# Kernel optimization log

Measured on AMD Instinct MI355X. Metric: run time of the kernel, lower is better.

Reference implementation:

```python
import jax, jax.numpy as jnp
import numpy as np

EPS = 1e-5

def _act_quant(x):
    # per-token int8 absmax quantization with straight-through estimator
    scale = 127.0 / jnp.clip(jnp.max(jnp.abs(x), axis=-1, keepdims=True), EPS, None)
    q = jnp.clip(jnp.round(x * scale), -128.0, 127.0) / scale
    return x + jax.lax.stop_gradient(q - x)

def _weight_quant(w):
    # per-tensor ternary (1.58-bit) quantization with STE
    scale = 1.0 / jnp.clip(jnp.mean(jnp.abs(w)), EPS, None)
    q = jnp.clip(jnp.round(w * scale), -1.0, 1.0) / scale
    return w + jax.lax.stop_gradient(q - w)

def _bitlinear(x, w, b):
    y = jnp.einsum('bsd,od->bso', _act_quant(x), _weight_quant(w))
    return y + b

def setup_inputs() -> dict:
    key = jax.random.key(0)
    k1, k2, k3, k4, k5 = jax.random.split(key, 5)
    B, S, D, F = 8, 4096, 1024, 3072
    return {
        'x': jax.random.normal(k1, (B, S, D), dtype=jnp.float32),
        'up_w': jax.random.normal(k2, (F, D), dtype=jnp.float32) * 0.125,
        'up_b': jax.random.normal(k3, (F,), dtype=jnp.float32) * 0.01,
        'down_w': jax.random.normal(k4, (D, F), dtype=jnp.float32) * 0.125,
        'down_b': jax.random.normal(k5, (D,), dtype=jnp.float32) * 0.01,
    }

def reference(x, up_w, up_b, down_w, down_b):
    hidden = _bitlinear(x, up_w, up_b)          # [B,S,3072]
    hidden = jnp.square(jax.nn.relu(hidden))    # relu(h)^2
    return _bitlinear(hidden, down_w, down_b)   # [B,S,1024]
```

## Files before the change

kernel.cpp:

```cpp
#include <hip/hip_runtime.h>
#include <hip/hip_bf16.h>
#include <stdint.h>

#define EPS 1e-5f

typedef int v4i __attribute__((ext_vector_type(4)));
typedef int v16i __attribute__((ext_vector_type(16)));
typedef const __attribute__((address_space(1))) void g_void;
typedef __attribute__((address_space(3))) void l_void;

__device__ inline float block_max_nw(float v, int nw) {
    __shared__ float s[8];
#pragma unroll
    for (int o = 32; o; o >>= 1) v = fmaxf(v, __shfl_xor(v, o, 64));
    if ((threadIdx.x & 63) == 0) s[threadIdx.x >> 6] = v;
    __syncthreads();
    float m = s[0];
    for (int i = 1; i < nw; ++i) m = fmaxf(m, s[i]);
    return m;
}

__device__ inline float block_sum64x4(float v) {
    __shared__ float s[4];
#pragma unroll
    for (int o = 32; o; o >>= 1) v += __shfl_xor(v, o, 64);
    if ((threadIdx.x & 63) == 0) s[threadIdx.x >> 6] = v;
    __syncthreads();
    return s[0] + s[1] + s[2] + s[3];
}

__global__ __launch_bounds__(256) void abs_sum_part_k(const float4* __restrict__ w,
                                                      int n4, float* __restrict__ part) {
    float s = 0.0f;
    for (int i = blockIdx.x * 256 + threadIdx.x; i < n4; i += 1024 * 256) {
        float4 v = w[i];
        s += fabsf(v.x) + fabsf(v.y) + fabsf(v.z) + fabsf(v.w);
    }
    s = block_sum64x4(s);
    if (threadIdx.x == 0) part[blockIdx.x] = s;
}

__global__ __launch_bounds__(256) void abs_sum_final_k(const float* __restrict__ parts,
                                                       float* __restrict__ sums) {
    const float* p = parts + blockIdx.x * 1024;
    const int t = threadIdx.x;
    float s = p[t] + p[t + 256] + p[t + 512] + p[t + 768];
    s = block_sum64x4(s);
    if (t == 0) sums[blockIdx.x] = s;
}

__global__ __launch_bounds__(256) void wquant_k(const float4* __restrict__ w,
                                                char4* __restrict__ q,
                                                const float* __restrict__ sum) {
    const float mean = fmaxf(sum[0] * (1.0f / 3145728.0f), EPS);
    const float scale = 1.0f / mean;
    const int i = blockIdx.x * 256 + threadIdx.x;
    float4 v = w[i];
    char4 c;
    c.x = (signed char)(int)fmaxf(fminf(rintf(v.x * scale), 1.0f), -1.0f);
    c.y = (signed char)(int)fmaxf(fminf(rintf(v.y * scale), 1.0f), -1.0f);
    c.z = (signed char)(int)fmaxf(fminf(rintf(v.z * scale), 1.0f), -1.0f);
    c.w = (signed char)(int)fmaxf(fminf(rintf(v.w * scale), 1.0f), -1.0f);
    q[i] = c;
}

__global__ __launch_bounds__(256) void aquant_k(const float4* __restrict__ x,
                                                char4* __restrict__ q,
                                                float* __restrict__ deq) {
    const int row = blockIdx.x, t = threadIdx.x;
    const float4 v = x[(size_t)row * 256 + t];
    float m = fmaxf(fmaxf(fabsf(v.x), fabsf(v.y)), fmaxf(fabsf(v.z), fabsf(v.w)));
    m = block_max_nw(m, 4);
    const float mc = fmaxf(m, EPS);
    const float sc = 127.0f / mc;
    char4 c;
    c.x = (signed char)(int)fmaxf(fminf(rintf(v.x * sc), 127.0f), -128.0f);
    c.y = (signed char)(int)fmaxf(fminf(rintf(v.y * sc), 127.0f), -128.0f);
    c.z = (signed char)(int)fmaxf(fminf(rintf(v.z * sc), 127.0f), -128.0f);
    c.w = (signed char)(int)fmaxf(fminf(rintf(v.w * sc), 127.0f), -128.0f);
    q[(size_t)row * 256 + t] = c;
    if (t == 0) deq[row] = mc / 127.0f;
}

__global__ __launch_bounds__(384) void hquant_k(unsigned short* __restrict__ hid,
                                                float* __restrict__ deq) {
    const size_t row = blockIdx.x;
    const int t = threadIdx.x;
    unsigned short* rp = hid + row * 3072;
    const uint4 u = ((const uint4*)rp)[t];
    float v[8];
    {
        uint32_t uu[4] = {u.x, u.y, u.z, u.w};
#pragma unroll
        for (int i = 0; i < 4; ++i) {
            uint32_t lo = uu[i] << 16, hi = uu[i] & 0xFFFF0000u;
            v[2 * i]     = __uint_as_float(lo);
            v[2 * i + 1] = __uint_as_float(hi);
        }
    }
    float m = 0.0f;
#pragma unroll
    for (int i = 0; i < 8; ++i) m = fmaxf(m, fabsf(v[i]));
    m = block_max_nw(m, 6);
    const float mc = fmaxf(m, EPS);
    const float sc = 127.0f / mc;
    uint32_t p0 = 0, p1 = 0;
#pragma unroll
    for (int i = 0; i < 4; ++i) {
        int c = (int)fminf(rintf(v[i] * sc), 127.0f);
        p0 |= (uint32_t)(c & 255) << (8 * i);
    }
#pragma unroll
    for (int i = 0; i < 4; ++i) {
        int c = (int)fminf(rintf(v[4 + i] * sc), 127.0f);
        p1 |= (uint32_t)(c & 255) << (8 * i);
    }
    uint2 pk; pk.x = p0; pk.y = p1;
    ((uint2*)rp)[t] = pk;
    if (t == 0) deq[row] = mc / 127.0f;
}

template <bool RELU2, typename OutT>
__global__ __launch_bounds__(512, 2) void gemm_i8(
    const int8_t* __restrict__ A, int lda,
    const int8_t* __restrict__ B, int ldb,
    OutT* __restrict__ O, int ldo,
    const float* __restrict__ rowDeq,
    const float* __restrict__ sumPtr,
    const float* __restrict__ bias,
    int K, int nTiles) {
    __shared__ __align__(16) char As[2][32768];
    __shared__ __align__(16) char Bs[2][32768];
    const int t = threadIdx.x;
    const int lane = t & 63;
    const int w = t >> 6;
    const int wm = w >> 2;
    const int wn = w & 3;
    const int xcd = blockIdx.x & 7;
    const int sb = blockIdx.x >> 3;
    const int bm = xcd + 8 * (sb / nTiles);
    const int bn = sb % nTiles;
    const long m0 = (long)bm * 256;
    const long n0 = (long)bn * 256;

    v16i acc[4][2];
#pragma unroll
    for (int i = 0; i < 4; ++i)
#pragma unroll
        for (int j = 0; j < 2; ++j) acc[i][j] = (v16i)(0);

    const int r32 = lane & 31;
    const int h = lane >> 5;
    const int swz = r32 & 7;
    const int srow = lane >> 3;
    const int scol = ((lane & 7) ^ srow) * 16;
    const int mloc = wm * 128;
    const int nloc = wn * 64;

    const int8_t* pa = A + (m0 + w * 8 + srow) * (long)lda + scol;
    const int8_t* pb = B + (n0 + w * 8 + srow) * (long)ldb + scol;

    int cs[4];
#pragma unroll
    for (int ks = 0; ks < 4; ++ks) cs[ks] = ((ks * 2 + h) ^ swz) * 16;

    const int NT = K >> 7;

    auto STAGE = [&](int tt, int buf) {
        const long ko = (long)tt << 7;
#pragma unroll
        for (int r = 0; r < 4; ++r)
            __builtin_amdgcn_global_load_lds((g_void*)(pa + (long)(r * 64) * lda + ko),
                                             (l_void*)(As[buf] + r * 8192 + w * 1024), 16, 0, 0);
#pragma unroll
        for (int r = 0; r < 4; ++r)
            __builtin_amdgcn_global_load_lds((g_void*)(pb + (long)(r * 64) * ldb + ko),
                                             (l_void*)(Bs[buf] + r * 8192 + w * 1024), 16, 0, 0);
    };

    STAGE(0, 0);
    STAGE(1, 1);
    asm volatile("s_waitcnt vmcnt(8)" ::: "memory");
    __builtin_amdgcn_s_barrier();
    asm volatile("" ::: "memory");

    for (int tt = 0; tt < NT; ++tt) {
        const int cur = tt & 1;
        v4i af[4][4], bf[2][4];
#pragma unroll
        for (int ks = 0; ks < 4; ++ks) {
#pragma unroll
            for (int mt = 0; mt < 4; ++mt)
                af[mt][ks] = *(const v4i*)(As[cur] + (mloc + mt * 32 + r32) * 128 + cs[ks]);
#pragma unroll
            for (int nt = 0; nt < 2; ++nt)
                bf[nt][ks] = *(const v4i*)(Bs[cur] + (nloc + nt * 32 + r32) * 128 + cs[ks]);
        }
        asm volatile("s_waitcnt lgkmcnt(0)" ::: "memory");
        __builtin_amdgcn_s_barrier();
        asm volatile("" ::: "memory");
        const bool pf = (tt + 2 < NT);
        if (pf) STAGE(tt + 2, cur);
        __builtin_amdgcn_s_setprio(1);
#pragma unroll
        for (int ks = 0; ks < 4; ++ks)
#pragma unroll
            for (int mt = 0; mt < 4; ++mt)
#pragma unroll
                for (int nt = 0; nt < 2; ++nt)
                    acc[mt][nt] = __builtin_amdgcn_mfma_i32_32x32x32_i8(
                        af[mt][ks], bf[nt][ks], acc[mt][nt], 0, 0, 0);
        __builtin_amdgcn_s_setprio(0);
        if (pf) asm volatile("s_waitcnt vmcnt(8)" ::: "memory");
        else    asm volatile("s_waitcnt vmcnt(0)" ::: "memory");
        __builtin_amdgcn_s_barrier();
        asm volatile("" ::: "memory");
    }

    const float wdeq = fmaxf(sumPtr[0] * (1.0f / 3145728.0f), EPS);
#pragma unroll
    for (int mt = 0; mt < 4; ++mt) {
#pragma unroll
        for (int g = 0; g < 4; ++g) {
#pragma unroll
            for (int rr = 0; rr < 4; ++rr) {
                const long row = m0 + mloc + mt * 32 + g * 8 + h * 4 + rr;
                const float rs = rowDeq[row] * wdeq;
#pragma unroll
                for (int nt = 0; nt < 2; ++nt) {
                    const long col = n0 + nloc + nt * 32 + r32;
                    float val = (float)acc[mt][nt][g * 4 + rr] * rs + bias[col];
                    if (RELU2) {
                        val = fmaxf(val, 0.0f);
                        val = val * val;
                    }
                    O[row * (long)ldo + col] = (OutT)val;
                }
            }
        }
    }
}

extern "C" void kernel_launch(void* const* d_in, const int* in_sizes, int n_in,
                              void* d_out, int out_size, void* d_ws, size_t ws_size,
                              hipStream_t stream) {
    const float* x      = (const float*)d_in[0];
    const float* up_w   = (const float*)d_in[1];
    const float* up_b   = (const float*)d_in[2];
    const float* down_w = (const float*)d_in[3];
    const float* down_b = (const float*)d_in[4];

    char* ws = (char*)d_ws;
    float*  sums   = (float*)ws;
    float*  parts  = (float*)(ws + 256);
    int8_t* qw_dn  = (int8_t*)(ws + 256 + 8192);
    float*  deqh   = (float*)(ws + 256 + 8192 + 3145728);
    __hip_bfloat16* hidden = (__hip_bfloat16*)(ws + 256 + 8192 + 3145728 + 131072);

    int8_t* qx    = (int8_t*)d_out;
    int8_t* qw_up = qx + 33554432;
    float*  deqx  = (float*)(qx + 33554432 + 3145728);

    abs_sum_part_k<<<1024, 256, 0, stream>>>((const float4*)up_w, 786432, parts);
    abs_sum_part_k<<<1024, 256, 0, stream>>>((const float4*)down_w, 786432, parts + 1024);
    abs_sum_final_k<<<2, 256, 0, stream>>>(parts, sums);

    wquant_k<<<3072, 256, 0, stream>>>((const float4*)up_w, (char4*)qw_up, &sums[0]);
    wquant_k<<<3072, 256, 0, stream>>>((const float4*)down_w, (char4*)qw_dn, &sums[1]);
    aquant_k<<<32768, 256, 0, stream>>>((const float4*)x, (char4*)qx, deqx);

    gemm_i8<true, __hip_bfloat16><<<1536, 512, 0, stream>>>(
        qx, 1024, qw_up, 1024, hidden, 3072, deqx, &sums[0], up_b, 1024, 12);
    hquant_k<<<32768, 384, 0, stream>>>((unsigned short*)hidden, deqh);
    gemm_i8<false, float><<<512, 512, 0, stream>>>(
        (const int8_t*)hidden, 6144, qw_dn, 3072, (float*)d_out, 1024,
        deqh, &sums[1], down_b, 3072, 4);
}
```

Before: 582.3 us.

## Switch int8 GEMM to 4-stage K=64 pipeline with single barrier per step

Changes the int8 GEMM main loop from double-buffered K=128 tiles to four LDS buffers of K=64 tiles, issuing the prefetch three stages ahead. The LDS layout and XOR swizzle are redone for 64-byte rows. The mid-iteration barrier after the LDS reads is dropped, so each step has only one barrier. The aim is deeper latency hiding of global loads and less synchronisation. The cost is twice as many loop iterations, with less MFMA work between barriers.

```diff
diff --git a/kernel.cpp b/kernel.cpp
--- a/kernel.cpp
+++ b/kernel.cpp
@@ -129,8 +129,8 @@
     const float* __restrict__ sumPtr,
     const float* __restrict__ bias,
     int K, int nTiles) {
-    __shared__ __align__(16) char As[2][32768];
-    __shared__ __align__(16) char Bs[2][32768];
+    __shared__ __align__(16) char As[4][16384];
+    __shared__ __align__(16) char Bs[4][16384];
     const int t = threadIdx.x;
     const int lane = t & 63;
     const int w = t >> 6;
@@ -151,59 +151,63 @@
 
     const int r32 = lane & 31;
     const int h = lane >> 5;
-    const int swz = r32 & 7;
-    const int srow = lane >> 3;
-    const int scol = ((lane & 7) ^ srow) * 16;
-    const int mloc = wm * 128;
-    const int nloc = wn * 64;
-
-    const int8_t* pa = A + (m0 + w * 8 + srow) * (long)lda + scol;
-    const int8_t* pb = B + (n0 + w * 8 + srow) * (long)ldb + scol;
-
-    int cs[4];
-#pragma unroll
-    for (int ks = 0; ks < 4; ++ks) cs[ks] = ((ks * 2 + h) ^ swz) * 16;
-
-    const int NT = K >> 7;
-
-    auto STAGE = [&](int tt, int buf) {
-        const long ko = (long)tt << 7;
-#pragma unroll
-        for (int r = 0; r < 4; ++r)
-            __builtin_amdgcn_global_load_lds((g_void*)(pa + (long)(r * 64) * lda + ko),
-                                             (l_void*)(As[buf] + r * 8192 + w * 1024), 16, 0, 0);
-#pragma unroll
-        for (int r = 0; r < 4; ++r)
-            __builtin_amdgcn_global_load_lds((g_void*)(pb + (long)(r * 64) * ldb + ko),
-                                             (l_void*)(Bs[buf] + r * 8192 + w * 1024), 16, 0, 0);
+
+    const int srow = lane >> 2;
+    const int sc = ((lane & 3) ^ ((lane >> 3) & 3)) * 16;
+    const int8_t* pa  = A + (m0 + 32 * w + srow) * (long)lda + sc;
+    const int8_t* pb  = B + (n0 + 32 * w + srow) * (long)ldb + sc;
+    const int8_t* pa1 = pa + 16 * (long)lda;
+    const int8_t* pb1 = pb + 16 * (long)ldb;
+    const int sdst = w * 2048;
+
+    int cro[2];
+#pragma unroll
+    for (int ks = 0; ks < 2; ++ks) cro[ks] = ((2 * ks + h) ^ ((r32 >> 1) & 3)) * 16;
+    const int arow = (wm * 128 + r32) * 64;
+    const int brow = (wn * 64 + r32) * 64;
+
+    const int NT = K >> 6;
+
+    auto STAGE = [&](int tt) {
+        const int buf = tt & 3;
+        const long ko = (long)tt << 6;
+        __builtin_amdgcn_global_load_lds((g_void*)(pa + ko),
+                                         (l_void*)(As[buf] + sdst), 16, 0, 0);
+        __builtin_amdgcn_global_load_lds((g_void*)(pa1 + ko),
+                                         (l_void*)(As[buf] + sdst + 1024), 16, 0, 0);
+        __builtin_amdgcn_global_load_lds((g_void*)(pb + ko),
+                                         (l_void*)(Bs[buf] + sdst), 16, 0, 0);
+        __builtin_amdgcn_global_load_lds((g_void*)(pb1 + ko),
+                                         (l_void*)(Bs[buf] + sdst + 1024), 16, 0, 0);
     };
 
-    STAGE(0, 0);
-    STAGE(1, 1);
+    STAGE(0);
+    STAGE(1);
+    STAGE(2);
     asm volatile("s_waitcnt vmcnt(8)" ::: "memory");
     __builtin_amdgcn_s_barrier();
-    asm volatile("" ::: "memory");
+    __builtin_amdgcn_sched_barrier(0);
 
     for (int tt = 0; tt < NT; ++tt) {
-        const int cur = tt & 1;
-        v4i af[4][4], bf[2][4];
-#pragma unroll
-        for (int ks = 0; ks < 4; ++ks) {
-#pragma unroll
-            for (int mt = 0; mt < 4; ++mt)
-                af[mt][ks] = *(const v4i*)(As[cur] + (mloc + mt * 32 + r32) * 128 + cs[ks]);
-#pragma unroll
-            for (int nt = 0; nt < 2; ++nt)
-                bf[nt][ks] = *(const v4i*)(Bs[cur] + (nloc + nt * 32 + r32) * 128 + cs[ks]);
-        }
-        asm volatile("s_waitcnt lgkmcnt(0)" ::: "memory");
-        __builtin_amdgcn_s_barrier();
-        asm volatile("" ::: "memory");
-        const bool pf = (tt + 2 < NT);
-        if (pf) STAGE(tt + 2, cur);
+        const char* ab = As[tt & 3];
+        const char* bb = Bs[tt & 3];
+        if (tt + 3 < NT) STAGE(tt + 3);
+
+        v4i af[4][2], bf[2][2];
+#pragma unroll
+        for (int mt = 0; mt < 4; ++mt)
+#pragma unroll
+            for (int ks = 0; ks < 2; ++ks)
+                af[mt][ks] = *(const v4i*)(ab + arow + mt * 2048 + cro[ks]);
+#pragma unroll
+        for (int nt = 0; nt < 2; ++nt)
+#pragma unroll
+            for (int ks = 0; ks < 2; ++ks)
+                bf[nt][ks] = *(const v4i*)(bb + brow + nt * 2048 + cro[ks]);
+
         __builtin_amdgcn_s_setprio(1);
 #pragma unroll
-        for (int ks = 0; ks < 4; ++ks)
+        for (int ks = 0; ks < 2; ++ks)
 #pragma unroll
             for (int mt = 0; mt < 4; ++mt)
 #pragma unroll
@@ -211,10 +215,12 @@
                     acc[mt][nt] = __builtin_amdgcn_mfma_i32_32x32x32_i8(
                         af[mt][ks], bf[nt][ks], acc[mt][nt], 0, 0, 0);
         __builtin_amdgcn_s_setprio(0);
-        if (pf) asm volatile("s_waitcnt vmcnt(8)" ::: "memory");
-        else    asm volatile("s_waitcnt vmcnt(0)" ::: "memory");
+
+        if (tt + 3 < NT)      asm volatile("s_waitcnt vmcnt(8)" ::: "memory");
+        else if (tt + 2 < NT) asm volatile("s_waitcnt vmcnt(4)" ::: "memory");
+        else                  asm volatile("s_waitcnt vmcnt(0)" ::: "memory");
         __builtin_amdgcn_s_barrier();
-        asm volatile("" ::: "memory");
+        __builtin_amdgcn_sched_barrier(0);
     }
 
     const float wdeq = fmaxf(sumPtr[0] * (1.0f / 3145728.0f), EPS);
@@ -224,11 +230,11 @@
         for (int g = 0; g < 4; ++g) {
 #pragma unroll
             for (int rr = 0; rr < 4; ++rr) {
-                const long row = m0 + mloc + mt * 32 + g * 8 + h * 4 + rr;
+                const long row = m0 + wm * 128 + mt * 32 + g * 8 + h * 4 + rr;
                 const float rs = rowDeq[row] * wdeq;
 #pragma unroll
                 for (int nt = 0; nt < 2; ++nt) {
-                    const long col = n0 + nloc + nt * 32 + r32;
+                    const long col = n0 + wn * 64 + nt * 32 + r32;
                     float val = (float)acc[mt][nt][g * 4 + rr] * rs + bias[col];
                     if (RELU2) {
                         val = fmaxf(val, 0.0f);
```

Measured after the change: 588.9 us. Within noise of the previous version (+1.1%).
